# Performance work log

Hardware: AMD Instinct MI355X
Metric: run time of the kernel (lower is better)

## Reference

```python
import jax, jax.numpy as jnp
import numpy as np

GAMMAS = (0.01, 0.1, 1.0, 10.0, 100.0)
FOCAL_GAMMA = 2.0
SMOOTH = 0.1
TASK_W = (0.4, 0.3, 0.3)
A_RECON, A_ORTH, A_ADV = 1.0, 0.1, 0.1
NUM_DOMAINS = 4
NUM_LABELS1 = 4


def focal_smooth(logits, targets, maskf):
    # FocalLoss.forward with smoothing > 0, masked mean
    n_classes = logits.shape[1]
    log_p = jax.nn.log_softmax(logits, axis=1)
    p = jnp.exp(log_p)
    onehot = jax.nn.one_hot(targets, n_classes, dtype=logits.dtype)
    smooth = onehot * (1.0 - SMOOTH) + SMOOTH / n_classes
    ce = -(smooth * log_p).sum(axis=1)
    pt = jnp.take_along_axis(p, targets[:, None], axis=1)[:, 0]
    loss = ce * (1.0 - pt) ** FOCAL_GAMMA
    return (loss * maskf).sum() / jnp.maximum(maskf.sum(), 1.0)


def ce_masked(logits, targets, maskf):
    log_p = jax.nn.log_softmax(logits, axis=1)
    nll = -jnp.take_along_axis(log_p, targets[:, None], axis=1)[:, 0]
    return (nll * maskf).sum() / jnp.maximum(maskf.sum(), 1.0)


def cond_mmd(feats, domains, labels, maskf):
    # Global pairwise sq-distance matrix; multi-gamma RBF kernels summed.
    sq = (feats ** 2).sum(axis=-1)                      # (B,)
    Dmat = sq[:, None] + sq[None, :] - 2.0 * feats @ feats.T  # (B,B)
    Ksum = jnp.zeros_like(Dmat)
    for g in GAMMAS:
        Ksum = Ksum + jnp.exp(-g * Dmat)
    loss = jnp.asarray(0.0, feats.dtype)
    count = jnp.asarray(0.0, feats.dtype)
    for lab in range(NUM_LABELS1):
        lm = (labels == lab).astype(feats.dtype) * maskf
        for d1 in range(NUM_DOMAINS):
            m1 = lm * (domains == d1).astype(feats.dtype)
            n1 = m1.sum()
            Km1 = Ksum @ m1
            for d2 in range(d1 + 1, NUM_DOMAINS):
                m2 = lm * (domains == d2).astype(feats.dtype)
                n2 = m2.sum()
                valid = (n1 > 1) & (n2 > 1)
                term = (m1 @ Km1) / jnp.maximum(n1, 1.0) ** 2 \
                     + (m2 @ (Ksum @ m2)) / jnp.maximum(n2, 1.0) ** 2 \
                     - 2.0 * (m2 @ Km1) / jnp.maximum(n1 * n2, 1.0)
                loss = loss + jnp.where(valid, term, 0.0)
                count = count + valid.astype(feats.dtype)
    return loss / jnp.maximum(count, 1.0)


def hsic(c, s):
    n = c.shape[0]
    c = c / jnp.maximum(jnp.linalg.norm(c, axis=-1, keepdims=True), 1e-12)
    s = s / jnp.maximum(jnp.linalg.norm(s, axis=-1, keepdims=True), 1e-12)
    K = c @ c.T
    L = s @ s.T
    Kc = K - K.mean(axis=0, keepdims=True) - K.mean(axis=1, keepdims=True) + K.mean()
    Lc = L - L.mean(axis=0, keepdims=True) - L.mean(axis=1, keepdims=True) + L.mean()
    return (Kc * Lc).sum() / (n - 1) ** 2


def setup_inputs() -> dict:
    key = jax.random.key(0)
    ks = jax.random.split(key, 20)
    B, D, H = 4096, 256, 768
    inp = {
        'logits1': jax.random.normal(ks[0], (B, 4), jnp.float32),
        'labels1': jax.random.randint(ks[1], (B,), 0, 4),
        'logits2': jax.random.normal(ks[2], (B, 6), jnp.float32),
        'labels2': jax.random.randint(ks[3], (B,), 0, 6),
        'logits3': jax.random.normal(ks[4], (B, 3), jnp.float32),
        'labels3': jax.random.randint(ks[5], (B,), 0, 3),
        'c_v': jax.random.normal(ks[6], (B, D), jnp.float32),
        's_v': jax.random.normal(ks[7], (B, D), jnp.float32),
        'c_t': jax.random.normal(ks[8], (B, D), jnp.float32),
        's_t': jax.random.normal(ks[9], (B, D), jnp.float32),
        'v_sv': jax.random.normal(ks[10], (B, NUM_DOMAINS), jnp.float32),
        'v_st': jax.random.normal(ks[11], (B, NUM_DOMAINS), jnp.float32),
        'domain_labels': jax.random.randint(ks[12], (B,), 0, NUM_DOMAINS),
        'mask': jnp.ones((B,), dtype=bool),
        'h_img_recon': jax.random.normal(ks[13], (B, H), jnp.float32),
        'h_img_orig': jax.random.normal(ks[14], (B, H), jnp.float32),
        'h_txt_recon': jax.random.normal(ks[15], (B, H), jnp.float32),
        'h_txt_orig': jax.random.normal(ks[16], (B, H), jnp.float32),
    }
    return inp


def reference(logits1, labels1, logits2, labels2, logits3, labels3,
              c_v, s_v, c_t, s_t, v_sv, v_st, domain_labels, mask,
              h_img_recon, h_img_orig, h_txt_recon, h_txt_orig):
    maskf = mask.astype(jnp.float32)
    total = jnp.asarray(0.0, jnp.float32)
    # classification (focal + label smoothing), per-task weighted
    total = total + TASK_W[0] * focal_smooth(logits1, labels1, maskf)
    total = total + TASK_W[1] * focal_smooth(logits2, labels2, maskf)
    total = total + TASK_W[2] * focal_smooth(logits3, labels3, maskf)
    # adversarial: CE on spurious domain logits + conditional MMD on causal feats
    l_adv_s = ce_masked(v_sv, domain_labels, maskf) + ce_masked(v_st, domain_labels, maskf)
    l_adv_c = cond_mmd(c_v, domain_labels, labels1, maskf) \
            + cond_mmd(c_t, domain_labels, labels1, maskf)
    total = total + A_ADV * (l_adv_s + l_adv_c)
    # orthogonality (HSIC), on unmasked features as in source
    l_orth = hsic(c_v, s_v) + hsic(c_t, s_t)
    total = total + A_ORTH * l_orth
    # reconstruction MSE
    l_recon = jnp.mean((h_img_recon - h_img_orig) ** 2) + jnp.mean((h_txt_recon - h_txt_orig) ** 2)
    total = total + A_RECON * l_recon
    return total
```

## Files before the change

kernel.cpp:

```cpp
#include <hip/hip_runtime.h>
#include <hip/hip_bf16.h>


typedef short bf16x8 __attribute__((ext_vector_type(8)));
typedef float f32x4 __attribute__((ext_vector_type(4)));
typedef unsigned long long u64;
typedef unsigned int u32;

static constexpr int D = 256;
static constexpr int H = 768;
static constexpr int NG = 16;
static constexpr float FX32 = 4294967296.f;
static constexpr float IFX32 = 2.3283064365386963e-10f;

__device__ inline void gAddFx(u64* p, float v) {
  long long q = (long long)llroundf(v * FX32);
  atomicAdd(p, (u64)q);
}
__device__ inline float fxToF(u64 v) { return (float)(long long)v * IFX32; }

__device__ inline float focal_n(const float* x, int n, int tgt,
                                float s_over_n, float oms) {
  float mx = x[0];
  for (int c = 1; c < n; ++c) mx = fmaxf(mx, x[c]);
  float se = 0.f, sx = 0.f;
  for (int c = 0; c < n; ++c) { se += __expf(x[c] - mx); sx += x[c]; }
  float logZ = mx + __logf(se);
  float ce = logZ - oms * x[tgt] - s_over_n * sx;
  float pt = __expf(x[tgt] - logZ);
  float om = 1.f - pt;
  return ce * om * om;
}

extern "C" __global__ __launch_bounds__(256) void k_pre(
    const void* __restrict__ mask, const int* __restrict__ y1,
    const int* __restrict__ dom,
    const float* __restrict__ l1, const float* __restrict__ l2,
    const float* __restrict__ l3, const int* __restrict__ y2,
    const int* __restrict__ y3,
    const float* __restrict__ vsv, const float* __restrict__ vst,
    const float* __restrict__ cv, const float* __restrict__ sv,
    const float* __restrict__ ct, const float* __restrict__ st,
    const float* __restrict__ ir, const float* __restrict__ io,
    const float* __restrict__ trc, const float* __restrict__ to,
    u64* SA, u64* GCU, u64* U64,
    int* gid, float* sq, float* inv, unsigned short* bf, u32* CNTB,
    int B, int N4, int NA, int NB) {
  __shared__ u32 sh3[3];
  __shared__ u32 cnt[17];
  __shared__ int redi[4];
  __shared__ float redf[4];
  int bid = blockIdx.x;
  int t = threadIdx.x;

  if (bid < NA) {
    if (t < 3) sh3[t] = 0;
    if (t < 17) cnt[t] = 0;
    __syncthreads();
    u32 a = 0, b2 = 0, cd = 0;
    if (t * 16 + 15 < B) {
      uint4 wv = ((const uint4*)mask)[t];
      u32 ws[4] = {wv.x, wv.y, wv.z, wv.w};
      #pragma unroll
      for (int j = 0; j < 4; ++j) {
        a |= ws[j] & 0xffu; b2 |= ws[j] & 0xff00u; cd |= ws[j] & 0xffff0000u;
      }
    }
    if (a) atomicOr(&sh3[0], 1u);
    if (b2) atomicOr(&sh3[1], 1u);
    if (cd) atomicOr(&sh3[2], 1u);
    __syncthreads();
    int mode;
    if ((sh3[1] | sh3[2]) == 0) mode = 0;
    else if (sh3[0] == 0 && sh3[1] == 0) mode = 1;
    else mode = 2;
    int r = bid * 256 + t;
    int mi = 0;
    float s[5] = {0.f, 0.f, 0.f, 0.f, 0.f};
    if (r < B) {
      if (mode == 0)      mi = ((const int*)mask)[r] ? 1 : 0;
      else if (mode == 1) mi = (((const float*)mask)[r] != 0.f) ? 1 : 0;
      else                mi = ((const unsigned char*)mask)[r] ? 1 : 0;
      int g = -1;
      if (mi) { g = y1[r] * 4 + dom[r]; atomicAdd(&cnt[g], 1u); }
      else atomicAdd(&cnt[16], 1u);
      gid[r] = g;
      if (mi) {
        float x[6];
        for (int c = 0; c < 4; ++c) x[c] = l1[r * 4 + c];
        s[0] = focal_n(x, 4, y1[r], 0.1f / 4.f, 0.9f);
        for (int c = 0; c < 6; ++c) x[c] = l2[r * 6 + c];
        s[1] = focal_n(x, 6, y2[r], 0.1f / 6.f, 0.9f);
        for (int c = 0; c < 3; ++c) x[c] = l3[r * 3 + c];
        s[2] = focal_n(x, 3, y3[r], 0.1f / 3.f, 0.9f);
        int d = dom[r];
        for (int c = 0; c < 4; ++c) x[c] = vsv[r * 4 + c];
        {
          float mx = fmaxf(fmaxf(x[0], x[1]), fmaxf(x[2], x[3]));
          float se = __expf(x[0]-mx)+__expf(x[1]-mx)+__expf(x[2]-mx)+__expf(x[3]-mx);
          s[3] = mx + __logf(se) - x[d];
        }
        for (int c = 0; c < 4; ++c) x[c] = vst[r * 4 + c];
        {
          float mx = fmaxf(fmaxf(x[0], x[1]), fmaxf(x[2], x[3]));
          float se = __expf(x[0]-mx)+__expf(x[1]-mx)+__expf(x[2]-mx)+__expf(x[3]-mx);
          s[4] = mx + __logf(se) - x[d];
        }
      }
    }
    int v = mi;
    #pragma unroll
    for (int o = 32; o > 0; o >>= 1) v += __shfl_down(v, o);
    if ((t & 63) == 0) redi[t >> 6] = v;
    __syncthreads();
    if (t == 0) atomicAdd(&SA[5], (u64)(redi[0] + redi[1] + redi[2] + redi[3]));
    if (t < NG && cnt[t]) atomicAdd(&GCU[t], (u64)cnt[t]);
    if (t < 17) CNTB[bid * 17 + t] = cnt[t];
    for (int k = 0; k < 5; ++k) {
      float x = s[k];
      #pragma unroll
      for (int o = 32; o > 0; o >>= 1) x += __shfl_down(x, o);
      __syncthreads();
      if ((t & 63) == 0) redf[t >> 6] = x;
      __syncthreads();
      if (t == 0) gAddFx(&SA[k], redf[0] + redf[1] + redf[2] + redf[3]);
    }
  } else if (bid < NA + NB) {
    int b = bid - NA;
    int f = b >> 6;
    int rb = b & 63;
    const float* p = (f == 0) ? cv : (f == 1) ? sv : (f == 2) ? ct : st;
    int w = t >> 6, L = t & 63;
    float up0 = 0.f, up1 = 0.f, up2 = 0.f, up3 = 0.f;
    for (int k = 0; k < 16; ++k) {
      int r = rb * 64 + w * 16 + k;
      float4 v = ((const float4*)(p + (size_t)r * D))[L];
      float ss = v.x * v.x + v.y * v.y + v.z * v.z + v.w * v.w;
      #pragma unroll
      for (int o = 32; o > 0; o >>= 1) ss += __shfl_down(ss, o);
      ss = __shfl(ss, 0);
      float iv = 1.f / fmaxf(sqrtf(ss), 1e-12f);
      if ((f & 1) == 0) {
        int fi = f >> 1;
        alignas(8) __hip_bfloat16 hb[4];
        hb[0] = __float2bfloat16(v.x); hb[1] = __float2bfloat16(v.y);
        hb[2] = __float2bfloat16(v.z); hb[3] = __float2bfloat16(v.w);
        *(uint2*)(bf + ((size_t)fi * B + r) * D + L * 4) = *(uint2*)hb;
        if (L == 0) sq[fi * B + r] = ss;
      }
      if (L == 0) inv[f * B + r] = iv;
      up0 += v.x * iv; up1 += v.y * iv; up2 += v.z * iv; up3 += v.w * iv;
    }
    u64* Uf = U64 + f * D + 4 * L;
    gAddFx(Uf + 0, up0); gAddFx(Uf + 1, up1);
    gAddFx(Uf + 2, up2); gAddFx(Uf + 3, up3);
  } else {
    int cidx = bid - (NA + NB);
    int j = cidx >> 8;
    int cb = cidx & 255;
    const float4* A  = (const float4*)(j ? trc : ir);
    const float4* Bp = (const float4*)(j ? to : io);
    float acc = 0.f;
    for (int idx = cb * 256 + t; idx < N4; idx += 256 * 256) {
      float4 a = A[idx], b = Bp[idx];
      float dx = a.x-b.x, dy = a.y-b.y, dz = a.z-b.z, dw = a.w-b.w;
      acc += dx*dx + dy*dy + dz*dz + dw*dw;
    }
    #pragma unroll
    for (int o = 32; o > 0; o >>= 1) acc += __shfl_down(acc, o);
    if ((t & 63) == 0) redf[t >> 6] = acc;
    __syncthreads();
    if (t == 0) gAddFx(&SA[6 + j], redf[0] + redf[1] + redf[2] + redf[3]);
  }
}

extern "C" __global__ __launch_bounds__(256) void k_sort(
    const u32* __restrict__ CNTB, const int* __restrict__ gid,
    const float* __restrict__ sq, int* __restrict__ perm,
    float* __restrict__ sqp, int* __restrict__ OFF, int B, int NA) {
  __shared__ int lg[256];
  __shared__ u32 cbs[17], tots[17];
  int b = blockIdx.x, t = threadIdx.x;
  if (t < 17) {
    u32 cb = 0, tot = 0;
    for (int b2 = 0; b2 < NA; ++b2) {
      u32 c = CNTB[b2 * 17 + t];
      cb += (b2 < b) ? c : 0u;
      tot += c;
    }
    cbs[t] = cb; tots[t] = tot;
  }
  int r = b * 256 + t;
  int g = 16;
  if (r < B) { int gg = gid[r]; g = (gg < 0) ? 16 : gg; }
  lg[t] = g;
  __syncthreads();
  if (b == 0 && t < 18) {
    u32 bb = 0;
    for (int g2 = 0; g2 < t; ++g2) bb += tots[g2];
    OFF[t] = (int)bb;
  }
  if (r < B) {
    u32 base = 0;
    for (int g2 = 0; g2 < g; ++g2) base += tots[g2];
    int rank = 0;
    for (int t2 = 0; t2 < t; ++t2) rank += (lg[t2] == g) ? 1 : 0;
    int pos = (int)(base + cbs[g]) + rank;
    perm[pos] = r;
    sqp[pos] = sq[r];
    sqp[B + pos] = sq[B + r];
  }
}

extern "C" __global__ __launch_bounds__(256) void k_big(
    const float* __restrict__ cv, const float* __restrict__ sv,
    const float* __restrict__ ct, const float* __restrict__ st,
    const float* __restrict__ inv, u64* M64,
    const unsigned short* __restrict__ bf, const float* __restrict__ sqp,
    const int* __restrict__ perm, const int* __restrict__ OFF,
    u64* GSP, int B) {
  __shared__ __align__(16) char smem[17536];
  int bid = blockIdx.x;
  int tid = threadIdx.x;

  if (bid < 512) {
    float (*lc)[16] = (float(*)[16])smem;
    float* lis = (float*)(smem + 16384);
    int p = bid >> 8;
    int a0 = ((bid >> 4) & 15) * 16;
    int i0 = (bid & 15) * 256;
    const float* c = p ? ct : cv;
    const float* s = p ? st : sv;
    const float* ic = inv + (2 * p) * B;
    const float* is = inv + (2 * p + 1) * B;
    int t = tid;
    if (t < 256) lis[t] = is[i0 + t];
    for (int e = t; e < 256 * 16; e += 256) {
      int i = e >> 4, rr = e & 15;
      lc[i][rr] = c[(size_t)(i0 + i) * D + a0 + rr] * ic[i0 + i];
    }
    __syncthreads();
    float4 acc[4];
    #pragma unroll
    for (int r = 0; r < 4; ++r) acc[r] = make_float4(0.f, 0.f, 0.f, 0.f);
    #pragma unroll 8
    for (int i = 0; i < 256; ++i) {
      float svv = s[(size_t)(i0 + i) * D + t] * lis[i];
      const float4* lr = (const float4*)lc[i];
      #pragma unroll
      for (int r = 0; r < 4; ++r) {
        float4 c4 = lr[r];
        acc[r].x += c4.x * svv; acc[r].y += c4.y * svv;
        acc[r].z += c4.z * svv; acc[r].w += c4.w * svv;
      }
    }
    u64* Mp = M64 + (size_t)p * D * D;
    #pragma unroll
    for (int r = 0; r < 4; ++r) {
      gAddFx(&Mp[(a0 + 4 * r + 0) * D + t], acc[r].x);
      gAddFx(&Mp[(a0 + 4 * r + 1) * D + t], acc[r].y);
      gAddFx(&Mp[(a0 + 4 * r + 2) * D + t], acc[r].z);
      gAddFx(&Mp[(a0 + 4 * r + 3) * D + t], acc[r].w);
    }
    return;
  }

  unsigned short* Ab = (unsigned short*)smem;
  unsigned short* Bb = (unsigned short*)(smem + 8192);
  float* sA = (float*)(smem + 16384);
  float* sB = (float*)(smem + 16640);
  int*   pA = (int*)(smem + 16896);
  int*   pB = (int*)(smem + 17152);
  int*   offs = (int*)(smem + 17408);

  int idx2 = bid - 512;
  int feat = idx2 & 1;
  int tlin = idx2 >> 1;
  int NT = B / 64;
  float tf = (float)tlin;
  int ti = (int)((2.f * NT + 1.f -
                  sqrtf((2.f * NT + 1.f) * (2.f * NT + 1.f) - 8.f * tf)) * 0.5f);
  while (ti > 0 && (ti * NT - (ti * (ti - 1)) / 2) > tlin) --ti;
  while (((ti + 1) * NT - ((ti + 1) * ti) / 2) <= tlin) ++ti;
  int tj = ti + (tlin - (ti * NT - (ti * (ti - 1)) / 2));
  int i0 = ti * 64, j0 = tj * 64;
  bool diag = (ti == tj);
  const unsigned short* fb = bf + (size_t)feat * B * D;
  const float* sqf = sqp + (size_t)feat * B;

  int w = tid >> 6, L = tid & 63, m = L & 15, q = L >> 4;

  if (tid < 64) { pA[tid] = perm[i0 + tid]; sA[tid] = sqf[i0 + tid]; }
  else if (tid < 128) { int r = tid - 64; pB[r] = perm[j0 + r]; sB[r] = sqf[j0 + r]; }
  else if (tid < 146) offs[tid - 128] = OFF[tid - 128];
  __syncthreads();

  int gr0 = 0, nbr = 0, gc0 = 0, ncb = 0;
  #pragma unroll
  for (int g = 1; g <= 17; ++g) {
    int o = offs[g];
    gr0 += (o <= i0) ? 1 : 0;
    nbr += (o > i0 && o < i0 + 64) ? 1 : 0;
    gc0 += (o <= j0) ? 1 : 0;
    ncb += (o > j0 && o < j0 + 64) ? 1 : 0;
  }
  if (gr0 == 16 || gc0 == 16) return;
  int gr1 = gr0 + nbr;
  int gc1 = gc0 + ncb;
  int s_r = nbr ? offs[gr1] : i0 + 64;
  int s_c = ncb ? offs[gc1] : j0 + 64;

  f32x4 acc[4] = {{0.f,0.f,0.f,0.f},{0.f,0.f,0.f,0.f},
                  {0.f,0.f,0.f,0.f},{0.f,0.f,0.f,0.f}};

  for (int hq = 0; hq < 4; ++hq) {
    if (hq) __syncthreads();
    for (int e = tid; e < 512; e += 256) {
      int row = e >> 3, ck = e & 7;
      uint4 v = *(const uint4*)(fb + (size_t)pA[row] * D + hq * 64 + ck * 8);
      *(uint4*)&Ab[row * 64 + ((ck ^ (row & 7)) * 8)] = v;
    }
    if (!diag) {
      for (int e = tid; e < 512; e += 256) {
        int row = e >> 3, ck = e & 7;
        uint4 v = *(const uint4*)(fb + (size_t)pB[row] * D + hq * 64 + ck * 8);
        *(uint4*)&Bb[row * 64 + ((ck ^ (row & 7)) * 8)] = v;
      }
    }
    __syncthreads();
    const unsigned short* Bp = diag ? Ab : Bb;
    int ar = w * 16 + m;
    #pragma unroll
    for (int kk = 0; kk < 2; ++kk) {
      bf16x8 aF = *(const bf16x8*)&Ab[ar * 64 + (((kk * 4 + q) ^ (ar & 7)) * 8)];
      #pragma unroll
      for (int c = 0; c < 4; ++c) {
        int br = c * 16 + m;
        bf16x8 bF = *(const bf16x8*)&Bp[br * 64 + (((kk * 4 + q) ^ (br & 7)) * 8)];
        acc[c] = __builtin_amdgcn_mfma_f32_16x16x32_bf16(aF, bF, acc[c], 0, 0, 0);
      }
    }
  }

  int ri0 = w * 16 + q * 4;
  u64* gsp = GSP + ((size_t)(tlin & 63) * 2 + feat) * NG * NG;

  if (nbr <= 1 && ncb <= 1) {
    float siv[4]; bool rhiv[4];
    #pragma unroll
    for (int v = 0; v < 4; ++v) {
      siv[v] = sA[ri0 + v];
      rhiv[v] = (i0 + ri0 + v) >= s_r;
    }
    float a00 = 0.f, a01 = 0.f, a10 = 0.f, a11 = 0.f;
    #pragma unroll
    for (int c = 0; c < 4; ++c) {
      int rj = c * 16 + m;
      float sb = sB[rj];
      float lo = 0.f, hi = 0.f;
      #pragma unroll
      for (int v = 0; v < 4; ++v) {
        float d = fmaxf(siv[v] + sb - 2.f * acc[c][v], 0.f);
        float K = __expf(-0.01f * d) + __expf(-0.1f * d) + __expf(-d)
                + __expf(-10.f * d) + __expf(-100.f * d);
        if (diag) {
          int ri = ri0 + v;
          K = (ri > rj) ? 0.f : (ri == rj) ? 5.f : K;
        }
        float kh = rhiv[v] ? K : 0.f;
        hi += kh; lo += K - kh;
      }
      bool chi = (j0 + rj) >= s_c;
      float loH = chi ? lo : 0.f;
      float hiH = chi ? hi : 0.f;
      a00 += lo - loH; a01 += loH;
      a10 += hi - hiH; a11 += hiH;
    }
    #pragma unroll
    for (int o = 32; o > 0; o >>= 1) {
      a00 += __shfl_down(a00, o); a01 += __shfl_down(a01, o);
      a10 += __shfl_down(a10, o); a11 += __shfl_down(a11, o);
    }
    if (L == 0) {
      if (a00 != 0.f)
        atomicAdd(&gsp[gr0 * NG + gc0], (u64)(long long)llroundf(a00 * 65536.f));
      if (a01 != 0.f && gc1 < 16)
        atomicAdd(&gsp[gr0 * NG + gc1], (u64)(long long)llroundf(a01 * 65536.f));
      if (a10 != 0.f && gr1 < 16)
        atomicAdd(&gsp[gr1 * NG + gc0], (u64)(long long)llroundf(a10 * 65536.f));
      if (a11 != 0.f && gr1 < 16 && gc1 < 16)
        atomicAdd(&gsp[gr1 * NG + gc1], (u64)(long long)llroundf(a11 * 65536.f));
    }
  } else {
    int giv[4]; float siv[4];
    #pragma unroll
    for (int v = 0; v < 4; ++v) {
      int idx = i0 + ri0 + v;
      int g = 0;
      #pragma unroll
      for (int k = 1; k <= 16; ++k) g += (offs[k] <= idx) ? 1 : 0;
      giv[v] = g;
      siv[v] = sA[ri0 + v];
    }
    #pragma unroll
    for (int c = 0; c < 4; ++c) {
      int rj = c * 16 + m;
      int jdx = j0 + rj;
      int gj = 0;
      #pragma unroll
      for (int k = 1; k <= 16; ++k) gj += (offs[k] <= jdx) ? 1 : 0;
      float sb = sB[rj];
      #pragma unroll
      for (int v = 0; v < 4; ++v) {
        int ri = ri0 + v;
        if (giv[v] < 16 && gj < 16 && !(diag && ri > rj)) {
          float K;
          if (diag && ri == rj) K = 5.f;
          else {
            float d = fmaxf(siv[v] + sb - 2.f * acc[c][v], 0.f);
            K = __expf(-0.01f * d) + __expf(-0.1f * d) + __expf(-d)
              + __expf(-10.f * d) + __expf(-100.f * d);
          }
          u32 kf = (u32)(K * 65536.f + 0.5f);
          atomicAdd(&gsp[giv[v] * NG + gj], (u64)kf);
        }
      }
    }
  }
}

extern "C" __global__ __launch_bounds__(256) void k_hsic(
    const u64* __restrict__ U64, const u64* __restrict__ M64, u64* SA) {
  __shared__ float red[8];
  __shared__ float ush[32], vsh[D];
  int p = blockIdx.y;
  int k0 = blockIdx.x * 32;
  int t = threadIdx.x;
  vsh[t] = fxToF(U64[(2 * p + 1) * D + t]);
  if (t < 32) ush[t] = fxToF(U64[(2 * p) * D + k0 + t]);
  __syncthreads();
  const u64* Mp = M64 + (size_t)p * D * D;
  float trkl = 0.f, cr = 0.f;
  #pragma unroll 4
  for (int k = 0; k < 32; ++k) {
    float mv = fxToF(Mp[(size_t)(k0 + k) * D + t]);
    trkl += mv * mv;
    cr += ush[k] * mv;
  }
  cr *= vsh[t];
  #pragma unroll
  for (int o = 32; o > 0; o >>= 1) { trkl += __shfl_down(trkl, o); cr += __shfl_down(cr, o); }
  if ((t & 63) == 0) { red[t >> 6] = trkl; red[4 + (t >> 6)] = cr; }
  __syncthreads();
  if (t == 0) gAddFx(&SA[10 + p], red[0] + red[1] + red[2] + red[3]);
  if (t == 64) gAddFx(&SA[12 + p], red[4] + red[5] + red[6] + red[7]);
}

extern "C" __global__ __launch_bounds__(256) void k_final(
    const u64* SA, const u64* GCU, const u64* GSP,
    const u64* U64, float* out, int B) {
  __shared__ float red[8];
  __shared__ float gssh[2 * NG * NG];
  int t = threadIdx.x;
  for (int e = t; e < 2 * NG * NG; e += 256) {
    u64 ssum = 0;
    int f = e >> 8, idx = e & 255;
    for (int cpy = 0; cpy < 64; ++cpy)
      ssum += GSP[((size_t)cpy * 2 + f) * NG * NG + idx];
    gssh[e] = (float)((double)ssum * (1.0 / 65536.0));
  }
  __syncthreads();

  float n = (float)B;
  float hs[2];
  for (int p = 0; p < 2; ++p) {
    float ut = fxToF(U64[(2 * p) * D + t]);
    float vt = fxToF(U64[(2 * p + 1) * D + t]);
    float uu = ut * ut, vv = vt * vt;
    #pragma unroll
    for (int o = 32; o > 0; o >>= 1) { uu += __shfl_down(uu, o); vv += __shfl_down(vv, o); }
    __syncthreads();
    if ((t & 63) == 0) { red[t >> 6] = uu; red[4 + (t >> 6)] = vv; }
    __syncthreads();
    float uus = red[0] + red[1] + red[2] + red[3];
    float vvs = red[4] + red[5] + red[6] + red[7];
    float trkl = (float)((double)(long long)SA[10 + p] * (double)IFX32);
    float cr   = (float)((double)(long long)SA[12 + p] * (double)IFX32);
    hs[p] = (trkl - (2.f / n) * cr + uus * vvs / (n * n))
          / ((n - 1.f) * (n - 1.f));
    __syncthreads();
  }
  if (t == 0) {
    float msum = fmaxf((float)SA[5], 1.f);
    float f1 = fxToF(SA[0]) / msum;
    float f2 = fxToF(SA[1]) / msum;
    float f3 = fxToF(SA[2]) / msum;
    float cesv = fxToF(SA[3]) / msum;
    float cest = fxToF(SA[4]) / msum;
    float mmd[2];
    for (int f = 0; f < 2; ++f) {
      float loss = 0.f, cntv = 0.f;
      for (int lab = 0; lab < 4; ++lab)
        for (int d1 = 0; d1 < 4; ++d1)
          for (int d2 = d1 + 1; d2 < 4; ++d2) {
            int a = lab * 4 + d1, b = lab * 4 + d2;
            float n1 = (float)GCU[a], n2 = (float)GCU[b];
            if (n1 > 1.f && n2 > 1.f) {
              float g11 = 2.f * gssh[f * 256 + a * NG + a] - 5.f * n1;
              float g22 = 2.f * gssh[f * 256 + b * NG + b] - 5.f * n2;
              float g12 = gssh[f * 256 + a * NG + b];
              loss += g11 / (fmaxf(n1, 1.f) * fmaxf(n1, 1.f))
                    + g22 / (fmaxf(n2, 1.f) * fmaxf(n2, 1.f))
                    - 2.f * g12 / fmaxf(n1 * n2, 1.f);
              cntv += 1.f;
            }
          }
      mmd[f] = loss / fmaxf(cntv, 1.f);
    }
    double rs = ((double)(long long)SA[6] + (double)(long long)SA[7])
              * (double)IFX32;
    float recon = (float)(rs / ((double)B * (double)H));
    float total = 0.4f * f1 + 0.3f * f2 + 0.3f * f3
                + 0.1f * (cesv + cest + mmd[0] + mmd[1])
                + 0.1f * (hs[0] + hs[1])
                + recon;
    out[0] = total;
  }
}

extern "C" void kernel_launch(void* const* d_in, const int* in_sizes, int n_in,
                              void* d_out, int out_size, void* d_ws, size_t ws_size,
                              hipStream_t stream) {
  const float* l1  = (const float*)d_in[0];
  const int*   y1  = (const int*)d_in[1];
  const float* l2  = (const float*)d_in[2];
  const int*   y2  = (const int*)d_in[3];
  const float* l3  = (const float*)d_in[4];
  const int*   y3  = (const int*)d_in[5];
  const float* cv  = (const float*)d_in[6];
  const float* sv  = (const float*)d_in[7];
  const float* ct  = (const float*)d_in[8];
  const float* st  = (const float*)d_in[9];
  const float* vsv = (const float*)d_in[10];
  const float* vst = (const float*)d_in[11];
  const int*   dom = (const int*)d_in[12];
  const void*  mask= d_in[13];
  const float* ir  = (const float*)d_in[14];
  const float* io  = (const float*)d_in[15];
  const float* trc = (const float*)d_in[16];
  const float* to  = (const float*)d_in[17];
  int B = in_sizes[1];

  u64* SA  = (u64*)d_ws;
  u64* GCU = SA + 32;
  u64* U64 = GCU + 16;
  u64* M64 = U64 + 4 * D;
  u64* GSP = M64 + 2 * D * D;
  u64* zend = GSP + 64 * 2 * NG * NG;
  size_t zeroBytes = (size_t)((char*)zend - (char*)d_ws);
  int*   gid = (int*)zend;
  float* sq  = (float*)(gid + B);
  float* inv = sq + 2 * B;
  unsigned short* bf = (unsigned short*)(inv + 4 * B);
  int*   perm = (int*)(bf + 2 * (size_t)B * D);
  float* sqp  = (float*)(perm + B);
  int*   OFF  = (int*)(sqp + 2 * B);
  u32*   CNTB = (u32*)(OFF + 18);

  int NA = B / 256;
  int NB = 4 * (B / 64);
  int NC = 512;
  int N4 = B * H / 4;

  hipMemsetAsync(d_ws, 0, zeroBytes, stream);
  k_pre<<<NA + NB + NC, 256, 0, stream>>>(
      mask, y1, dom, l1, l2, l3, y2, y3, vsv, vst,
      cv, sv, ct, st, ir, io, trc, to,
      SA, GCU, U64, gid, sq, inv, bf, CNTB, B, N4, NA, NB);
  k_sort<<<NA, 256, 0, stream>>>(CNTB, gid, sq, perm, sqp, OFF, B, NA);
  int NT = B / 64;
  int nmmd = 2 * (NT * (NT + 1) / 2);
  k_big<<<512 + nmmd, 256, 0, stream>>>(cv, sv, ct, st, inv, M64,
                                        bf, sqp, perm, OFF, GSP, B);
  k_hsic<<<dim3(8, 2), 256, 0, stream>>>(U64, M64, SA);
  k_final<<<1, 256, 0, stream>>>(SA, GCU, GSP, U64, (float*)d_out, B);
}
```

Measured before the change: 253.3 us.

## Compute HSIC cross-covariance with bf16 MFMA on transposed normalized features

Replaces the FP32 scalar cross-covariance (c^T s) blocks, which accumulated into a 64-bit fixed-point matrix with atomics, with a bf16 MFMA GEMM. A new mid kernel transposes and normalizes the four feature matrices to bf16. Each of the two K-halves writes its own fp32 partial matrix, and k_hsic sums the two halves, which removes the atomics and the memset of the M64 buffer. The sort kernel's per-thread rank scan is replaced with a wave ballot/popcount scheme merged into the same launch, and the MMD tile loads hoist their address computations. This trades precision (bf16 inputs) and extra workspace for the transposed data.

```diff
diff --git a/kernel.cpp b/kernel.cpp
--- a/kernel.cpp
+++ b/kernel.cpp
@@ -174,106 +174,156 @@
   }
 }
 
-extern "C" __global__ __launch_bounds__(256) void k_sort(
+extern "C" __global__ __launch_bounds__(256) void k_mid(
     const u32* __restrict__ CNTB, const int* __restrict__ gid,
-    const float* __restrict__ sq, int* __restrict__ perm,
-    float* __restrict__ sqp, int* __restrict__ OFF, int B, int NA) {
-  __shared__ int lg[256];
-  __shared__ u32 cbs[17], tots[17];
-  int b = blockIdx.x, t = threadIdx.x;
-  if (t < 17) {
-    u32 cb = 0, tot = 0;
-    for (int b2 = 0; b2 < NA; ++b2) {
-      u32 c = CNTB[b2 * 17 + t];
-      cb += (b2 < b) ? c : 0u;
-      tot += c;
-    }
-    cbs[t] = cb; tots[t] = tot;
-  }
-  int r = b * 256 + t;
-  int g = 16;
-  if (r < B) { int gg = gid[r]; g = (gg < 0) ? 16 : gg; }
-  lg[t] = g;
-  __syncthreads();
-  if (b == 0 && t < 18) {
-    u32 bb = 0;
-    for (int g2 = 0; g2 < t; ++g2) bb += tots[g2];
-    OFF[t] = (int)bb;
-  }
-  if (r < B) {
-    u32 base = 0;
-    for (int g2 = 0; g2 < g; ++g2) base += tots[g2];
-    int rank = 0;
-    for (int t2 = 0; t2 < t; ++t2) rank += (lg[t2] == g) ? 1 : 0;
-    int pos = (int)(base + cbs[g]) + rank;
-    perm[pos] = r;
-    sqp[pos] = sq[r];
-    sqp[B + pos] = sq[B + r];
-  }
-}
-
-extern "C" __global__ __launch_bounds__(256) void k_big(
+    const float* __restrict__ sq,
     const float* __restrict__ cv, const float* __restrict__ sv,
     const float* __restrict__ ct, const float* __restrict__ st,
-    const float* __restrict__ inv, u64* M64,
+    const float* __restrict__ inv,
+    int* __restrict__ perm, float* __restrict__ sqp, int* __restrict__ OFF,
+    unsigned short* __restrict__ bnT, int B, int NA) {
+  __shared__ float ld[64 * 65];
+  __shared__ u32 cbs[17], tots[17], wcnt[4][17];
+  __shared__ u32 base[18];
+  int b = blockIdx.x, t = threadIdx.x;
+
+  if (b < NA) {
+    if (t < 68) ((u32*)wcnt)[t] = 0;
+    if (t < 17) {
+      u32 cb = 0, tot = 0;
+      for (int b2 = 0; b2 < NA; ++b2) {
+        u32 c = CNTB[b2 * 17 + t];
+        cb += (b2 < b) ? c : 0u;
+        tot += c;
+      }
+      cbs[t] = cb; tots[t] = tot;
+    }
+    int r = b * 256 + t;
+    int g = 16;
+    if (r < B) { int gg = gid[r]; g = (gg < 0) ? 16 : gg; }
+    __syncthreads();
+    if (t == 0) {
+      u32 s = 0;
+      for (int g2 = 0; g2 < 17; ++g2) { base[g2] = s; s += tots[g2]; }
+      base[17] = s;
+    }
+    u64 msk = ~0ull;
+    #pragma unroll
+    for (int bit = 0; bit < 5; ++bit) {
+      int bv = (g >> bit) & 1;
+      u64 bl = __ballot(bv);
+      msk &= bv ? bl : ~bl;
+    }
+    int lane = t & 63, w = t >> 6;
+    int rwave = __popcll(msk & ((1ull << lane) - 1ull));
+    if (rwave == 0) wcnt[w][g] = (u32)__popcll(msk);
+    __syncthreads();
+    if (r < B) {
+      int rank = rwave;
+      for (int w2 = 0; w2 < 4; ++w2) if (w2 < w) rank += (int)wcnt[w2][g];
+      int pos = (int)(base[g] + cbs[g]) + rank;
+      perm[pos] = r;
+      sqp[pos] = sq[r];
+      sqp[B + pos] = sq[B + r];
+    }
+    if (b == 0 && t < 18) OFF[t] = (int)base[t];
+  } else {
+    int TPF = (B >> 6) * 4;
+    int tb = b - NA;
+    int fm = tb / TPF, tile = tb - fm * TPF;
+    int it = tile >> 2, at = tile & 3;
+    const float* src = (fm == 0) ? cv : (fm == 1) ? sv : (fm == 2) ? ct : st;
+    const float* ivf = inv + (size_t)fm * B;
+    int i0 = it * 64, a0 = at * 64;
+    for (int e = t; e < 1024; e += 256) {
+      int i = e >> 4, c4 = e & 15;
+      float4 v = ((const float4*)(src + (size_t)(i0 + i) * D))[at * 16 + c4];
+      float ivv = ivf[i0 + i];
+      ld[i * 65 + c4 * 4 + 0] = v.x * ivv;
+      ld[i * 65 + c4 * 4 + 1] = v.y * ivv;
+      ld[i * 65 + c4 * 4 + 2] = v.z * ivv;
+      ld[i * 65 + c4 * 4 + 3] = v.w * ivv;
+    }
+    __syncthreads();
+    unsigned short* dst = bnT + (size_t)fm * D * B;
+    for (int e = t; e < 512; e += 256) {
+      int a = e >> 3, ic = e & 7;
+      alignas(16) unsigned short h[8];
+      #pragma unroll
+      for (int j = 0; j < 8; ++j) {
+        __hip_bfloat16 hb = __float2bfloat16(ld[(ic * 8 + j) * 65 + a]);
+        h[j] = *(unsigned short*)&hb;
+      }
+      *(uint4*)(dst + (size_t)(a0 + a) * B + i0 + ic * 8) = *(uint4*)h;
+    }
+  }
+}
+
+extern "C" __global__ __launch_bounds__(256) void k_big(
     const unsigned short* __restrict__ bf, const float* __restrict__ sqp,
     const int* __restrict__ perm, const int* __restrict__ OFF,
+    const unsigned short* __restrict__ bnT, float* __restrict__ Mf32,
     u64* GSP, int B) {
   __shared__ __align__(16) char smem[17536];
+  unsigned short* Ab = (unsigned short*)smem;
+  unsigned short* Bb = (unsigned short*)(smem + 8192);
   int bid = blockIdx.x;
   int tid = threadIdx.x;
-
-  if (bid < 512) {
-    float (*lc)[16] = (float(*)[16])smem;
-    float* lis = (float*)(smem + 16384);
-    int p = bid >> 8;
-    int a0 = ((bid >> 4) & 15) * 16;
-    int i0 = (bid & 15) * 256;
-    const float* c = p ? ct : cv;
-    const float* s = p ? st : sv;
-    const float* ic = inv + (2 * p) * B;
-    const float* is = inv + (2 * p + 1) * B;
-    int t = tid;
-    if (t < 256) lis[t] = is[i0 + t];
-    for (int e = t; e < 256 * 16; e += 256) {
-      int i = e >> 4, rr = e & 15;
-      lc[i][rr] = c[(size_t)(i0 + i) * D + a0 + rr] * ic[i0 + i];
-    }
-    __syncthreads();
-    float4 acc[4];
-    #pragma unroll
-    for (int r = 0; r < 4; ++r) acc[r] = make_float4(0.f, 0.f, 0.f, 0.f);
-    #pragma unroll 8
-    for (int i = 0; i < 256; ++i) {
-      float svv = s[(size_t)(i0 + i) * D + t] * lis[i];
-      const float4* lr = (const float4*)lc[i];
-      #pragma unroll
-      for (int r = 0; r < 4; ++r) {
-        float4 c4 = lr[r];
-        acc[r].x += c4.x * svv; acc[r].y += c4.y * svv;
-        acc[r].z += c4.z * svv; acc[r].w += c4.w * svv;
-      }
-    }
-    u64* Mp = M64 + (size_t)p * D * D;
-    #pragma unroll
-    for (int r = 0; r < 4; ++r) {
-      gAddFx(&Mp[(a0 + 4 * r + 0) * D + t], acc[r].x);
-      gAddFx(&Mp[(a0 + 4 * r + 1) * D + t], acc[r].y);
-      gAddFx(&Mp[(a0 + 4 * r + 2) * D + t], acc[r].z);
-      gAddFx(&Mp[(a0 + 4 * r + 3) * D + t], acc[r].w);
+  int w = tid >> 6, L = tid & 63, m = L & 15, q = L >> 4;
+  int r0 = tid >> 3, ck = tid & 7;
+  int swz = (ck ^ (r0 & 7)) * 8;
+  int ar = w * 16 + m;
+
+  if (bid < 64) {
+    int half = bid & 1, bb = (bid >> 1) & 3, ab = (bid >> 3) & 3, p = (bid >> 5) & 1;
+    const unsigned short* Abase = bnT + (size_t)(2 * p) * D * B;
+    const unsigned short* Bbase = bnT + (size_t)(2 * p + 1) * D * B;
+    size_t kof = (size_t)half * (B >> 1) + ck * 8;
+    const uint4* gA0 = (const uint4*)(Abase + (size_t)(ab * 64 + r0) * B + kof);
+    const uint4* gA1 = (const uint4*)(Abase + (size_t)(ab * 64 + r0 + 32) * B + kof);
+    const uint4* gB0 = (const uint4*)(Bbase + (size_t)(bb * 64 + r0) * B + kof);
+    const uint4* gB1 = (const uint4*)(Bbase + (size_t)(bb * 64 + r0 + 32) * B + kof);
+    uint4* dA0 = (uint4*)&Ab[r0 * 64 + swz];
+    uint4* dA1 = (uint4*)&Ab[(r0 + 32) * 64 + swz];
+    uint4* dB0 = (uint4*)&Bb[r0 * 64 + swz];
+    uint4* dB1 = (uint4*)&Bb[(r0 + 32) * 64 + swz];
+    f32x4 acc[4] = {{0.f,0.f,0.f,0.f},{0.f,0.f,0.f,0.f},
+                    {0.f,0.f,0.f,0.f},{0.f,0.f,0.f,0.f}};
+    int nh = B >> 7;
+    for (int hq = 0; hq < nh; ++hq) {
+      *dA0 = gA0[hq * 8]; *dA1 = gA1[hq * 8];
+      *dB0 = gB0[hq * 8]; *dB1 = gB1[hq * 8];
+      __syncthreads();
+      #pragma unroll
+      for (int kk = 0; kk < 2; ++kk) {
+        bf16x8 aF = *(const bf16x8*)&Ab[ar * 64 + (((kk * 4 + q) ^ (ar & 7)) * 8)];
+        #pragma unroll
+        for (int c = 0; c < 4; ++c) {
+          int br = c * 16 + m;
+          bf16x8 bF = *(const bf16x8*)&Bb[br * 64 + (((kk * 4 + q) ^ (br & 7)) * 8)];
+          acc[c] = __builtin_amdgcn_mfma_f32_16x16x32_bf16(aF, bF, acc[c], 0, 0, 0);
+        }
+      }
+      if (hq < nh - 1) __syncthreads();
+    }
+    float* Mo = Mf32 + (size_t)(half * 2 + p) * D * D;
+    int ri0 = w * 16 + q * 4;
+    #pragma unroll
+    for (int c = 0; c < 4; ++c) {
+      #pragma unroll
+      for (int v = 0; v < 4; ++v)
+        Mo[(size_t)(ab * 64 + ri0 + v) * D + bb * 64 + c * 16 + m] = acc[c][v];
     }
     return;
   }
 
-  unsigned short* Ab = (unsigned short*)smem;
-  unsigned short* Bb = (unsigned short*)(smem + 8192);
   float* sA = (float*)(smem + 16384);
   float* sB = (float*)(smem + 16640);
   int*   pA = (int*)(smem + 16896);
   int*   pB = (int*)(smem + 17152);
   int*   offs = (int*)(smem + 17408);
 
-  int idx2 = bid - 512;
+  int idx2 = bid - 64;
   int feat = idx2 & 1;
   int tlin = idx2 >> 1;
   int NT = B / 64;
@@ -288,8 +338,6 @@
   const unsigned short* fb = bf + (size_t)feat * B * D;
   const float* sqf = sqp + (size_t)feat * B;
 
-  int w = tid >> 6, L = tid & 63, m = L & 15, q = L >> 4;
-
   if (tid < 64) { pA[tid] = perm[i0 + tid]; sA[tid] = sqf[i0 + tid]; }
   else if (tid < 128) { int r = tid - 64; pB[r] = perm[j0 + r]; sB[r] = sqf[j0 + r]; }
   else if (tid < 146) offs[tid - 128] = OFF[tid - 128];
@@ -310,26 +358,27 @@
   int s_r = nbr ? offs[gr1] : i0 + 64;
   int s_c = ncb ? offs[gc1] : j0 + 64;
 
+  const uint4* gA0 = (const uint4*)(fb + (size_t)pA[r0] * D + ck * 8);
+  const uint4* gA1 = (const uint4*)(fb + (size_t)pA[r0 + 32] * D + ck * 8);
+  uint4* dA0 = (uint4*)&Ab[r0 * 64 + swz];
+  uint4* dA1 = (uint4*)&Ab[(r0 + 32) * 64 + swz];
+  const uint4* gB0 = nullptr; const uint4* gB1 = nullptr;
+  uint4* dB0 = nullptr; uint4* dB1 = nullptr;
+  if (!diag) {
+    gB0 = (const uint4*)(fb + (size_t)pB[r0] * D + ck * 8);
+    gB1 = (const uint4*)(fb + (size_t)pB[r0 + 32] * D + ck * 8);
+    dB0 = (uint4*)&Bb[r0 * 64 + swz];
+    dB1 = (uint4*)&Bb[(r0 + 32) * 64 + swz];
+  }
+  const unsigned short* Bp = diag ? Ab : Bb;
+
   f32x4 acc[4] = {{0.f,0.f,0.f,0.f},{0.f,0.f,0.f,0.f},
                   {0.f,0.f,0.f,0.f},{0.f,0.f,0.f,0.f}};
 
   for (int hq = 0; hq < 4; ++hq) {
-    if (hq) __syncthreads();
-    for (int e = tid; e < 512; e += 256) {
-      int row = e >> 3, ck = e & 7;
-      uint4 v = *(const uint4*)(fb + (size_t)pA[row] * D + hq * 64 + ck * 8);
-      *(uint4*)&Ab[row * 64 + ((ck ^ (row & 7)) * 8)] = v;
-    }
-    if (!diag) {
-      for (int e = tid; e < 512; e += 256) {
-        int row = e >> 3, ck = e & 7;
-        uint4 v = *(const uint4*)(fb + (size_t)pB[row] * D + hq * 64 + ck * 8);
-        *(uint4*)&Bb[row * 64 + ((ck ^ (row & 7)) * 8)] = v;
-      }
-    }
-    __syncthreads();
-    const unsigned short* Bp = diag ? Ab : Bb;
-    int ar = w * 16 + m;
+    *dA0 = gA0[hq * 8]; *dA1 = gA1[hq * 8];
+    if (!diag) { *dB0 = gB0[hq * 8]; *dB1 = gB1[hq * 8]; }
+    __syncthreads();
     #pragma unroll
     for (int kk = 0; kk < 2; ++kk) {
       bf16x8 aF = *(const bf16x8*)&Ab[ar * 64 + (((kk * 4 + q) ^ (ar & 7)) * 8)];
@@ -340,6 +389,7 @@
         acc[c] = __builtin_amdgcn_mfma_f32_16x16x32_bf16(aF, bF, acc[c], 0, 0, 0);
       }
     }
+    if (hq < 3) __syncthreads();
   }
 
   int ri0 = w * 16 + q * 4;
@@ -430,7 +480,7 @@
 }
 
 extern "C" __global__ __launch_bounds__(256) void k_hsic(
-    const u64* __restrict__ U64, const u64* __restrict__ M64, u64* SA) {
+    const u64* __restrict__ U64, const float* __restrict__ Mf32, u64* SA) {
   __shared__ float red[8];
   __shared__ float ush[32], vsh[D];
   int p = blockIdx.y;
@@ -439,11 +489,12 @@
   vsh[t] = fxToF(U64[(2 * p + 1) * D + t]);
   if (t < 32) ush[t] = fxToF(U64[(2 * p) * D + k0 + t]);
   __syncthreads();
-  const u64* Mp = M64 + (size_t)p * D * D;
+  const float* M0 = Mf32 + (size_t)p * D * D;
+  const float* M1 = Mf32 + (size_t)(2 + p) * D * D;
   float trkl = 0.f, cr = 0.f;
   #pragma unroll 4
   for (int k = 0; k < 32; ++k) {
-    float mv = fxToF(Mp[(size_t)(k0 + k) * D + t]);
+    float mv = M0[(size_t)(k0 + k) * D + t] + M1[(size_t)(k0 + k) * D + t];
     trkl += mv * mv;
     cr += ush[k] * mv;
   }
@@ -554,15 +605,16 @@
   u64* SA  = (u64*)d_ws;
   u64* GCU = SA + 32;
   u64* U64 = GCU + 16;
-  u64* M64 = U64 + 4 * D;
-  u64* GSP = M64 + 2 * D * D;
+  u64* GSP = U64 + 4 * D;
   u64* zend = GSP + 64 * 2 * NG * NG;
   size_t zeroBytes = (size_t)((char*)zend - (char*)d_ws);
-  int*   gid = (int*)zend;
+  unsigned short* bf  = (unsigned short*)zend;
+  unsigned short* bnT = bf + 2 * (size_t)B * D;
+  float* Mf32 = (float*)(bnT + 4 * (size_t)D * B);
+  int*   gid = (int*)(Mf32 + 4 * (size_t)D * D);
   float* sq  = (float*)(gid + B);
   float* inv = sq + 2 * B;
-  unsigned short* bf = (unsigned short*)(inv + 4 * B);
-  int*   perm = (int*)(bf + 2 * (size_t)B * D);
+  int*   perm = (int*)(inv + 4 * B);
   float* sqp  = (float*)(perm + B);
   int*   OFF  = (int*)(sqp + 2 * B);
   u32*   CNTB = (u32*)(OFF + 18);
@@ -577,11 +629,12 @@
       mask, y1, dom, l1, l2, l3, y2, y3, vsv, vst,
       cv, sv, ct, st, ir, io, trc, to,
       SA, GCU, U64, gid, sq, inv, bf, CNTB, B, N4, NA, NB);
-  k_sort<<<NA, 256, 0, stream>>>(CNTB, gid, sq, perm, sqp, OFF, B, NA);
+  int NTR = B / 4;
+  k_mid<<<NA + NTR, 256, 0, stream>>>(CNTB, gid, sq, cv, sv, ct, st, inv,
+                                      perm, sqp, OFF, bnT, B, NA);
   int NT = B / 64;
   int nmmd = 2 * (NT * (NT + 1) / 2);
-  k_big<<<512 + nmmd, 256, 0, stream>>>(cv, sv, ct, st, inv, M64,
-                                        bf, sqp, perm, OFF, GSP, B);
-  k_hsic<<<dim3(8, 2), 256, 0, stream>>>(U64, M64, SA);
+  k_big<<<64 + nmmd, 256, 0, stream>>>(bf, sqp, perm, OFF, bnT, Mf32, GSP, B);
+  k_hsic<<<dim3(8, 2), 256, 0, stream>>>(U64, Mf32, SA);
   k_final<<<1, 256, 0, stream>>>(SA, GCU, GSP, U64, (float*)d_out, B);
 }
```

Result: faster. 222.3 us (-12.2%).
